# Optimization experiments

Measured on AMD Instinct MI355X. Metric: run time of the kernel, lower is better.

## Reference

```python
import jax, jax.numpy as jnp
import numpy as np

N_NODES = 50000
IN, HID, OUT = 128, 128, 47
N_EDGES = 800000


def _glorot(key, shape):
    fan_in, fan_out = shape[1], shape[0]
    lim = np.sqrt(6.0 / (fan_in + fan_out)).astype(np.float32)
    return jax.random.uniform(key, shape, jnp.float32, -lim, lim)


def setup_inputs() -> dict:
    key = jax.random.key(0)
    ks = jax.random.split(key, 12)
    x = jax.random.normal(ks[0], (N_NODES, IN), jnp.float32)
    src = jax.random.randint(ks[1], (N_EDGES,), 0, N_NODES)
    dst = jax.random.randint(ks[2], (N_EDGES,), 0, N_NODES)
    return {
        "x": x, "src": src, "dst": dst,
        "w_self1": _glorot(ks[3], (HID, IN)),  "w_neigh1": _glorot(ks[4], (HID, IN)),  "b1": jnp.zeros((HID,), jnp.float32),
        "w_self2": _glorot(ks[5], (HID, HID)), "w_neigh2": _glorot(ks[6], (HID, HID)), "b2": jnp.zeros((HID,), jnp.float32),
        "w_self3": _glorot(ks[7], (OUT, HID)), "w_neigh3": _glorot(ks[8], (OUT, HID)), "b3": jnp.zeros((OUT,), jnp.float32),
    }


def _sage_conv(h, src, dst, w_self, w_neigh, b):
    # gather src features, mean-reduce per dst node (DGL copy_u + mean)
    msg = h[src]                                                  # [E, d]
    agg = jax.ops.segment_sum(msg, dst, num_segments=N_NODES)    # [N, d]
    deg = jax.ops.segment_sum(jnp.ones((dst.shape[0],), h.dtype), dst, num_segments=N_NODES)
    mean = agg / jnp.maximum(deg, 1.0)[:, None]
    # DGL SAGEConv('mean'): fc_self(h_dst) + fc_neigh(h_neigh); bias on fc_self only
    return h @ w_self.T + b + mean @ w_neigh.T


def reference(x, src, dst,
              w_self1, w_neigh1, b1,
              w_self2, w_neigh2, b2,
              w_self3, w_neigh3, b3):
    h = _sage_conv(x, src, dst, w_self1, w_neigh1, b1)
    h = jax.nn.relu(h)  # dropout is identity in eval mode
    h = _sage_conv(h, src, dst, w_self2, w_neigh2, b2)
    h = jax.nn.relu(h)
    h = _sage_conv(h, src, dst, w_self3, w_neigh3, b3)
    return h
```

## Files before the change

kernel.cpp:

```cpp
#include <hip/hip_runtime.h>

#define N_NODES 50000
#define N_EDGES 800000
#define DIM 128
#define OUTD 47
#define NBK 196
#define EPB 4096
#define NBIN ((N_EDGES + EPB - 1) / EPB)
#define XCVT_NB (N_NODES * DIM / 8 / 256)
#define WCVT_NB (DIM + DIM + 48)

typedef __attribute__((ext_vector_type(8))) short v8s;
typedef __attribute__((ext_vector_type(8))) unsigned short v8u;
typedef __attribute__((ext_vector_type(4))) float v4f;
typedef __attribute__((ext_vector_type(2))) float v2f;

static __device__ __forceinline__ unsigned short f2bf(float f) {
    union { float f; unsigned int u; } v; v.f = f;
    unsigned int x = v.u;
    return (unsigned short)((x + 0x7fffu + ((x >> 16) & 1u)) >> 16);
}
static __device__ __forceinline__ unsigned char f2fp8(float f) {
    unsigned int pk = __builtin_amdgcn_cvt_pk_fp8_f32(f, f, 0, false);
    return (unsigned char)(pk & 0xffu);
}

__global__ __launch_bounds__(256) void k_prep(const float* __restrict__ x,
                                              unsigned short* __restrict__ xb,
                                              unsigned int* __restrict__ x8,
                                              const int* __restrict__ dst,
                                              int* __restrict__ parts,
                                              const float* __restrict__ ws1, const float* __restrict__ wn1,
                                              const float* __restrict__ ws2, const float* __restrict__ wn2,
                                              const float* __restrict__ ws3, const float* __restrict__ wn3,
                                              unsigned short* __restrict__ wb1,
                                              unsigned short* __restrict__ wb2,
                                              unsigned short* __restrict__ wb3) {
    __shared__ int hist[NBK];
    const int bx = blockIdx.x, tid = threadIdx.x;
    if (bx < XCVT_NB) {
        int i = bx * 256 + tid;
        float4 v0 = ((const float4*)x)[i * 2];
        float4 v1 = ((const float4*)x)[i * 2 + 1];
        ushort4 o0, o1;
        o0.x = f2bf(v0.x); o0.y = f2bf(v0.y); o0.z = f2bf(v0.z); o0.w = f2bf(v0.w);
        o1.x = f2bf(v1.x); o1.y = f2bf(v1.y); o1.z = f2bf(v1.z); o1.w = f2bf(v1.w);
        ((ushort4*)xb)[i * 2] = o0;
        ((ushort4*)xb)[i * 2 + 1] = o1;
        unsigned int a = __builtin_amdgcn_cvt_pk_fp8_f32(v0.x, v0.y, 0, false);
        a = __builtin_amdgcn_cvt_pk_fp8_f32(v0.z, v0.w, a, true);
        unsigned int b = __builtin_amdgcn_cvt_pk_fp8_f32(v1.x, v1.y, 0, false);
        b = __builtin_amdgcn_cvt_pk_fp8_f32(v1.z, v1.w, b, true);
        uint2 o; o.x = a; o.y = b;
        ((uint2*)x8)[i] = o;
    } else if (bx < XCVT_NB + NBIN) {
        const int j = bx - XCVT_NB;
        for (int i = tid; i < NBK; i += 256) hist[i] = 0;
        __syncthreads();
        const int e0 = j * EPB;
        const int ecnt = min(EPB, N_EDGES - e0);
        for (int r = tid; r < ecnt; r += 256)
            atomicAdd(&hist[dst[e0 + r] >> 8], 1);
        __syncthreads();
        for (int i = tid; i < NBK; i += 256) parts[j * NBK + i] = hist[i];
    } else {
        int b2 = bx - XCVT_NB - NBIN;
        const float *sw, *nw; unsigned short* ob; int j, J;
        if (b2 < DIM)            { sw = ws1; nw = wn1; ob = wb1; j = b2;            J = DIM; }
        else if (b2 < 2 * DIM)   { sw = ws2; nw = wn2; ob = wb2; j = b2 - DIM;      J = DIM; }
        else                     { sw = ws3; nw = wn3; ob = wb3; j = b2 - 2 * DIM;  J = OUTD; }
        int k = tid;
        float v = 0.f;
        if (j < J) v = (k < DIM) ? sw[j * DIM + k] : nw[j * DIM + (k - DIM)];
        ob[j * 256 + k] = f2bf(v);
    }
}

__global__ __launch_bounds__(256) void k_scan2(const int* __restrict__ parts,
                                               int* __restrict__ gbase,
                                               int* __restrict__ boffB,
                                               int* __restrict__ btot,
                                               int* __restrict__ row_ptr) {
    __shared__ int s[256];
    const int t = threadIdx.x;
    int tot = 0;
    if (t < NBK)
        for (int i = 0; i < NBIN; ++i) tot += parts[i * NBK + t];
    s[t] = tot;
    __syncthreads();
    for (int off = 1; off < 256; off <<= 1) {
        int u = (t >= off) ? s[t - off] : 0;
        __syncthreads();
        s[t] += u;
        __syncthreads();
    }
    if (t < NBK) {
        int run = s[t] - tot;
        boffB[t] = run; btot[t] = tot;
        for (int i = 0; i < NBIN; ++i) {
            gbase[i * NBK + t] = run;
            run += parts[i * NBK + t];
        }
    }
    if (t == 255) row_ptr[N_NODES] = s[255];
}

__global__ __launch_bounds__(256) void k_bin(const int* __restrict__ src,
                                             const int* __restrict__ dst,
                                             const int* __restrict__ gbase,
                                             unsigned int* __restrict__ packed) {
    __shared__ int gb[NBK], cnt[NBK];
    const int t = threadIdx.x;
    for (int i = t; i < NBK; i += 256) { gb[i] = gbase[blockIdx.x * NBK + i]; cnt[i] = 0; }
    __syncthreads();
    const int e0 = blockIdx.x * EPB;
    const int ecnt = min(EPB, N_EDGES - e0);
    for (int r = t; r < ecnt; r += 256) {
        int s = src[e0 + r], d = dst[e0 + r];
        int b = d >> 8;
        int loc = atomicAdd(&cnt[b], 1);
        packed[gb[b] + loc] = ((unsigned int)s << 8) | (unsigned int)(d & 255);
    }
}

__global__ __launch_bounds__(256) void k_place(const unsigned int* __restrict__ packed,
                                               const int* __restrict__ boffB,
                                               const int* __restrict__ btot,
                                               int* __restrict__ row_ptr,
                                               int* __restrict__ src_sorted) {
    __shared__ int hist[256], cur[256], s[256];
    const int b = blockIdx.x, t = threadIdx.x;
    hist[t] = 0;
    __syncthreads();
    const int base = boffB[b], cb = btot[b];
    for (int i = t; i < cb; i += 256)
        atomicAdd(&hist[packed[base + i] & 255u], 1);
    __syncthreads();
    int v = hist[t];
    s[t] = v;
    __syncthreads();
    for (int off = 1; off < 256; off <<= 1) {
        int u = (t >= off) ? s[t - off] : 0;
        __syncthreads();
        s[t] += u;
        __syncthreads();
    }
    int excl = base + s[t] - v;
    int node = b * 256 + t;
    if (node < N_NODES) row_ptr[node] = excl;
    cur[t] = excl;
    __syncthreads();
    for (int i = t; i < cb; i += 256) {
        unsigned int pkt = packed[base + i];
        int pos = atomicAdd(&cur[pkt & 255u], 1);
        src_sorted[pos] = (int)(pkt >> 8);
    }
}

__global__ __launch_bounds__(256) void k_agg8(const unsigned char* __restrict__ h8,
                                              const int* __restrict__ row_ptr,
                                              const int* __restrict__ srcs,
                                              unsigned short* __restrict__ meanb) {
    const int tid = threadIdx.x;
    const int lane = tid & 63, wv = tid >> 6;
    const int g = lane & 15, ns = lane >> 4;
    const int n = blockIdx.x * 16 + wv * 4 + ns;
    const int start = row_ptr[n], end = row_ptr[n + 1];
    float a0=0.f,a1=0.f,a2=0.f,a3=0.f,a4=0.f,a5=0.f,a6=0.f,a7=0.f;
    int e = start;
    for (; e + 2 <= end; e += 2) {
        int s0 = srcs[e], s1 = srcs[e + 1];
        uint2 u0 = *(const uint2*)(h8 + (size_t)s0 * DIM + g * 8);
        uint2 u1 = *(const uint2*)(h8 + (size_t)s1 * DIM + g * 8);
        v2f p0 = __builtin_amdgcn_cvt_pk_f32_fp8(u0.x, false);
        v2f p1 = __builtin_amdgcn_cvt_pk_f32_fp8(u0.x, true);
        v2f p2 = __builtin_amdgcn_cvt_pk_f32_fp8(u0.y, false);
        v2f p3 = __builtin_amdgcn_cvt_pk_f32_fp8(u0.y, true);
        v2f q0 = __builtin_amdgcn_cvt_pk_f32_fp8(u1.x, false);
        v2f q1 = __builtin_amdgcn_cvt_pk_f32_fp8(u1.x, true);
        v2f q2 = __builtin_amdgcn_cvt_pk_f32_fp8(u1.y, false);
        v2f q3 = __builtin_amdgcn_cvt_pk_f32_fp8(u1.y, true);
        a0 += p0[0] + q0[0]; a1 += p0[1] + q0[1];
        a2 += p1[0] + q1[0]; a3 += p1[1] + q1[1];
        a4 += p2[0] + q2[0]; a5 += p2[1] + q2[1];
        a6 += p3[0] + q3[0]; a7 += p3[1] + q3[1];
    }
    if (e < end) {
        int s0 = srcs[e];
        uint2 u0 = *(const uint2*)(h8 + (size_t)s0 * DIM + g * 8);
        v2f p0 = __builtin_amdgcn_cvt_pk_f32_fp8(u0.x, false);
        v2f p1 = __builtin_amdgcn_cvt_pk_f32_fp8(u0.x, true);
        v2f p2 = __builtin_amdgcn_cvt_pk_f32_fp8(u0.y, false);
        v2f p3 = __builtin_amdgcn_cvt_pk_f32_fp8(u0.y, true);
        a0 += p0[0]; a1 += p0[1]; a2 += p1[0]; a3 += p1[1];
        a4 += p2[0]; a5 += p2[1]; a6 += p3[0]; a7 += p3[1];
    }
    int d = end - start;
    float inv = (d > 0) ? 1.f / (float)d : 0.f;
    v8u o;
    o[0]=f2bf(a0*inv); o[1]=f2bf(a1*inv); o[2]=f2bf(a2*inv); o[3]=f2bf(a3*inv);
    o[4]=f2bf(a4*inv); o[5]=f2bf(a5*inv); o[6]=f2bf(a6*inv); o[7]=f2bf(a7*inv);
    *(v8u*)(meanb + (size_t)n * DIM + g * 8) = o;
}

template <int JT, int TPW, bool RELU, bool OUTBF>
__global__ __launch_bounds__(256) void k_gemm_lds(const unsigned short* __restrict__ Ab,
                                                  const unsigned short* __restrict__ Mb,
                                                  const unsigned short* __restrict__ Wb,
                                                  const float* __restrict__ bias,
                                                  void* __restrict__ out,
                                                  unsigned char* __restrict__ out8,
                                                  int outdim) {
    __shared__ unsigned short Alds[64 * 256];
    __shared__ unsigned short Wlds[JT * 256];
    const int tid = threadIdx.x;
    const int m0 = blockIdx.x * 64;
    const int j0 = blockIdx.y * JT;
    v8u ar[8];
    #pragma unroll
    for (int i = 0; i < 8; ++i) {
        int t = tid + 256 * i;
        int row = t >> 5, ch = t & 31;
        int node = m0 + row; if (node >= N_NODES) node = N_NODES - 1;
        const unsigned short* s = (ch < 16) ? (Ab + (size_t)node * DIM + ch * 8)
                                            : (Mb + (size_t)node * DIM + (ch - 16) * 8);
        ar[i] = *(const v8u*)s;
    }
    constexpr int WI = (JT * 32 + 255) / 256;
    v8u wr[WI];
    #pragma unroll
    for (int i = 0; i < WI; ++i) {
        int t = tid + 256 * i;
        if (t < JT * 32) {
            int row = t >> 5, ch = t & 31;
            wr[i] = *(const v8u*)(Wb + (size_t)(j0 + row) * 256 + ch * 8);
        }
    }
    #pragma unroll
    for (int i = 0; i < 8; ++i) {
        int t = tid + 256 * i;
        int row = t >> 5, ch = t & 31;
        *(v8u*)(Alds + row * 256 + ((ch * 8) ^ ((row & 7) * 8))) = ar[i];
    }
    #pragma unroll
    for (int i = 0; i < WI; ++i) {
        int t = tid + 256 * i;
        if (t < JT * 32) {
            int row = t >> 5, ch = t & 31;
            *(v8u*)(Wlds + row * 256 + ((ch * 8) ^ ((row & 7) * 8))) = wr[i];
        }
    }
    __syncthreads();
    const int lane = tid & 63, wv = tid >> 6;
    const int m = lane & 15, qd = lane >> 4;
    const int arow = wv * 16 + m;
    v4f acc[TPW] = {};
    #pragma unroll
    for (int c = 0; c < 8; ++c) {
        const int koff = c * 32 + qd * 8;
        v8s af = *(const v8s*)(Alds + arow * 256 + (koff ^ ((arow & 7) * 8)));
        #pragma unroll
        for (int t = 0; t < TPW; ++t) {
            int wrow = t * 16 + m;
            v8s wf = *(const v8s*)(Wlds + wrow * 256 + (koff ^ ((wrow & 7) * 8)));
            acc[t] = __builtin_amdgcn_mfma_f32_16x16x32_bf16(af, wf, acc[t], 0, 0, 0);
        }
    }
    #pragma unroll
    for (int t = 0; t < TPW; ++t) {
        int col = j0 + t * 16 + m;
        bool colok = (col < outdim);
        float bv = colok ? bias[col] : 0.f;
        #pragma unroll
        for (int r = 0; r < 4; ++r) {
            int nrow = m0 + wv * 16 + qd * 4 + r;
            if (colok && nrow < N_NODES) {
                float v = acc[t][r] + bv;
                if (RELU) v = fmaxf(v, 0.f);
                size_t idx = (size_t)nrow * outdim + col;
                if (OUTBF) {
                    ((unsigned short*)out)[idx] = f2bf(v);
                    out8[idx] = f2fp8(v);
                } else {
                    ((float*)out)[idx] = v;
                }
            }
        }
    }
}

extern "C" void kernel_launch(void* const* d_in, const int* in_sizes, int n_in,
                              void* d_out, int out_size, void* d_ws, size_t ws_size,
                              hipStream_t stream) {
    const float* x   = (const float*)d_in[0];
    const int*   src = (const int*)d_in[1];
    const int*   dst = (const int*)d_in[2];
    const float* ws1 = (const float*)d_in[3];
    const float* wn1 = (const float*)d_in[4];
    const float* b1  = (const float*)d_in[5];
    const float* ws2 = (const float*)d_in[6];
    const float* wn2 = (const float*)d_in[7];
    const float* b2  = (const float*)d_in[8];
    const float* ws3 = (const float*)d_in[9];
    const float* wn3 = (const float*)d_in[10];
    const float* b3  = (const float*)d_in[11];

    char* p = (char*)d_ws;
    auto alloc = [&](size_t bytes) { char* r = p; p += (bytes + 255) & ~(size_t)255; return r; };
    int*   row_ptr = (int*)alloc((size_t)(N_NODES + 1) * 4);
    int*   srcs    = (int*)alloc((size_t)N_EDGES * 4);
    unsigned int* packed = (unsigned int*)alloc((size_t)N_EDGES * 4);
    int*   parts   = (int*)alloc((size_t)NBIN * NBK * 4);
    int*   gbase   = (int*)alloc((size_t)NBIN * NBK * 4);
    int*   boffB   = (int*)alloc((size_t)NBK * 4);
    int*   btot    = (int*)alloc((size_t)NBK * 4);
    unsigned short* xb    = (unsigned short*)alloc((size_t)N_NODES * DIM * 2);
    unsigned short* meanb = (unsigned short*)alloc((size_t)N_NODES * DIM * 2);
    unsigned short* h1b   = (unsigned short*)alloc((size_t)N_NODES * DIM * 2);
    unsigned short* h2b   = (unsigned short*)alloc((size_t)N_NODES * DIM * 2);
    unsigned char*  h8    = (unsigned char*)alloc((size_t)N_NODES * DIM);
    unsigned short* wb1 = (unsigned short*)alloc((size_t)DIM * 256 * 2);
    unsigned short* wb2 = (unsigned short*)alloc((size_t)DIM * 256 * 2);
    unsigned short* wb3 = (unsigned short*)alloc((size_t)48 * 256 * 2);

    k_prep<<<XCVT_NB + NBIN + WCVT_NB, 256, 0, stream>>>(
        x, xb, (unsigned int*)h8, dst, parts,
        ws1, wn1, ws2, wn2, ws3, wn3, wb1, wb2, wb3);
    k_scan2<<<1, 256, 0, stream>>>(parts, gbase, boffB, btot, row_ptr);
    k_bin<<<NBIN, 256, 0, stream>>>(src, dst, gbase, packed);
    k_place<<<NBK, 256, 0, stream>>>(packed, boffB, btot, row_ptr, srcs);

    const int MB = (N_NODES + 63) / 64;
    const int AB = N_NODES / 16;

    k_agg8<<<AB, 256, 0, stream>>>(h8, row_ptr, srcs, meanb);
    k_gemm_lds<64, 4, true, true><<<dim3(MB, 2), 256, 0, stream>>>(xb, meanb, wb1, b1, h1b, h8, DIM);
    k_agg8<<<AB, 256, 0, stream>>>(h8, row_ptr, srcs, meanb);
    k_gemm_lds<64, 4, true, true><<<dim3(MB, 2), 256, 0, stream>>>(h1b, meanb, wb2, b2, h2b, h8, DIM);
    k_agg8<<<AB, 256, 0, stream>>>(h8, row_ptr, srcs, meanb);
    k_gemm_lds<48, 3, false, false><<<dim3(MB, 1), 256, 0, stream>>>(h2b, meanb, wb3, b3, d_out, nullptr, OUTD);
}
```

Baseline: 264.4 us.

## Fuse neighbor mean aggregation into per-layer GEMM kernel via LDS

Merges the separate aggregation kernel and the GEMM kernel into one per-layer kernel. Each block gathers and averages neighbor fp8 features for its 64 nodes straight into the LDS A-tile, then loops over output-column halves reloading weights. This removes the bf16 mean buffer write and readback and half the kernel launches, and uses ping-pong fp8 buffers because the fused kernel reads and writes h8 in the same launch. In exchange the grid drops from 3125 aggregation blocks to 782 blocks with less gather parallelism per block, and the gather is serialized before the MFMA phase.

```diff
diff --git a/kernel.cpp b/kernel.cpp
--- a/kernel.cpp
+++ b/kernel.cpp
@@ -157,132 +157,128 @@
     }
 }
 
-__global__ __launch_bounds__(256) void k_agg8(const unsigned char* __restrict__ h8,
-                                              const int* __restrict__ row_ptr,
-                                              const int* __restrict__ srcs,
-                                              unsigned short* __restrict__ meanb) {
-    const int tid = threadIdx.x;
-    const int lane = tid & 63, wv = tid >> 6;
-    const int g = lane & 15, ns = lane >> 4;
-    const int n = blockIdx.x * 16 + wv * 4 + ns;
-    const int start = row_ptr[n], end = row_ptr[n + 1];
-    float a0=0.f,a1=0.f,a2=0.f,a3=0.f,a4=0.f,a5=0.f,a6=0.f,a7=0.f;
-    int e = start;
-    for (; e + 2 <= end; e += 2) {
-        int s0 = srcs[e], s1 = srcs[e + 1];
-        uint2 u0 = *(const uint2*)(h8 + (size_t)s0 * DIM + g * 8);
-        uint2 u1 = *(const uint2*)(h8 + (size_t)s1 * DIM + g * 8);
-        v2f p0 = __builtin_amdgcn_cvt_pk_f32_fp8(u0.x, false);
-        v2f p1 = __builtin_amdgcn_cvt_pk_f32_fp8(u0.x, true);
-        v2f p2 = __builtin_amdgcn_cvt_pk_f32_fp8(u0.y, false);
-        v2f p3 = __builtin_amdgcn_cvt_pk_f32_fp8(u0.y, true);
-        v2f q0 = __builtin_amdgcn_cvt_pk_f32_fp8(u1.x, false);
-        v2f q1 = __builtin_amdgcn_cvt_pk_f32_fp8(u1.x, true);
-        v2f q2 = __builtin_amdgcn_cvt_pk_f32_fp8(u1.y, false);
-        v2f q3 = __builtin_amdgcn_cvt_pk_f32_fp8(u1.y, true);
-        a0 += p0[0] + q0[0]; a1 += p0[1] + q0[1];
-        a2 += p1[0] + q1[0]; a3 += p1[1] + q1[1];
-        a4 += p2[0] + q2[0]; a5 += p2[1] + q2[1];
-        a6 += p3[0] + q3[0]; a7 += p3[1] + q3[1];
-    }
-    if (e < end) {
-        int s0 = srcs[e];
-        uint2 u0 = *(const uint2*)(h8 + (size_t)s0 * DIM + g * 8);
-        v2f p0 = __builtin_amdgcn_cvt_pk_f32_fp8(u0.x, false);
-        v2f p1 = __builtin_amdgcn_cvt_pk_f32_fp8(u0.x, true);
-        v2f p2 = __builtin_amdgcn_cvt_pk_f32_fp8(u0.y, false);
-        v2f p3 = __builtin_amdgcn_cvt_pk_f32_fp8(u0.y, true);
-        a0 += p0[0]; a1 += p0[1]; a2 += p1[0]; a3 += p1[1];
-        a4 += p2[0]; a5 += p2[1]; a6 += p3[0]; a7 += p3[1];
-    }
-    int d = end - start;
-    float inv = (d > 0) ? 1.f / (float)d : 0.f;
-    v8u o;
-    o[0]=f2bf(a0*inv); o[1]=f2bf(a1*inv); o[2]=f2bf(a2*inv); o[3]=f2bf(a3*inv);
-    o[4]=f2bf(a4*inv); o[5]=f2bf(a5*inv); o[6]=f2bf(a6*inv); o[7]=f2bf(a7*inv);
-    *(v8u*)(meanb + (size_t)n * DIM + g * 8) = o;
-}
-
-template <int JT, int TPW, bool RELU, bool OUTBF>
-__global__ __launch_bounds__(256) void k_gemm_lds(const unsigned short* __restrict__ Ab,
-                                                  const unsigned short* __restrict__ Mb,
-                                                  const unsigned short* __restrict__ Wb,
-                                                  const float* __restrict__ bias,
-                                                  void* __restrict__ out,
-                                                  unsigned char* __restrict__ out8,
-                                                  int outdim) {
+template <int JH, int NH, int TPW, bool RELU, bool OUTBF>
+__global__ __launch_bounds__(256) void k_layer(const unsigned short* __restrict__ selfb,
+                                               const unsigned char* __restrict__ h8in,
+                                               const unsigned short* __restrict__ Wb,
+                                               const float* __restrict__ bias,
+                                               const int* __restrict__ row_ptr,
+                                               const int* __restrict__ srcs,
+                                               void* __restrict__ out,
+                                               unsigned char* __restrict__ out8,
+                                               int outdim) {
     __shared__ unsigned short Alds[64 * 256];
-    __shared__ unsigned short Wlds[JT * 256];
+    __shared__ unsigned short Wlds[JH * 256];
     const int tid = threadIdx.x;
     const int m0 = blockIdx.x * 64;
-    const int j0 = blockIdx.y * JT;
-    v8u ar[8];
     #pragma unroll
-    for (int i = 0; i < 8; ++i) {
+    for (int i = 0; i < 4; ++i) {
+        int t = tid + 256 * i;
+        int row = t >> 4, ch = t & 15;
+        int node = m0 + row; if (node >= N_NODES) node = N_NODES - 1;
+        v8u v = *(const v8u*)(selfb + (size_t)node * DIM + ch * 8);
+        *(v8u*)(Alds + row * 256 + ((ch * 8) ^ ((row & 7) * 8))) = v;
+    }
+    {
+        const int g = tid & 15, sl = tid >> 4;
+        for (int k = 0; k < 4; ++k) {
+            int row = sl * 4 + k;
+            int n = m0 + row;
+            float a0=0.f,a1=0.f,a2=0.f,a3=0.f,a4=0.f,a5=0.f,a6=0.f,a7=0.f;
+            int d = 0;
+            if (n < N_NODES) {
+                int start = row_ptr[n], end = row_ptr[n + 1];
+                d = end - start;
+                int e = start;
+                for (; e + 2 <= end; e += 2) {
+                    int s0 = srcs[e], s1 = srcs[e + 1];
+                    uint2 u0 = *(const uint2*)(h8in + (size_t)s0 * DIM + g * 8);
+                    uint2 u1 = *(const uint2*)(h8in + (size_t)s1 * DIM + g * 8);
+                    v2f p0 = __builtin_amdgcn_cvt_pk_f32_fp8(u0.x, false);
+                    v2f p1 = __builtin_amdgcn_cvt_pk_f32_fp8(u0.x, true);
+                    v2f p2 = __builtin_amdgcn_cvt_pk_f32_fp8(u0.y, false);
+                    v2f p3 = __builtin_amdgcn_cvt_pk_f32_fp8(u0.y, true);
+                    v2f q0 = __builtin_amdgcn_cvt_pk_f32_fp8(u1.x, false);
+                    v2f q1 = __builtin_amdgcn_cvt_pk_f32_fp8(u1.x, true);
+                    v2f q2 = __builtin_amdgcn_cvt_pk_f32_fp8(u1.y, false);
+                    v2f q3 = __builtin_amdgcn_cvt_pk_f32_fp8(u1.y, true);
+                    a0 += p0[0] + q0[0]; a1 += p0[1] + q0[1];
+                    a2 += p1[0] + q1[0]; a3 += p1[1] + q1[1];
+                    a4 += p2[0] + q2[0]; a5 += p2[1] + q2[1];
+                    a6 += p3[0] + q3[0]; a7 += p3[1] + q3[1];
+                }
+                if (e < end) {
+                    int s0 = srcs[e];
+                    uint2 u0 = *(const uint2*)(h8in + (size_t)s0 * DIM + g * 8);
+                    v2f p0 = __builtin_amdgcn_cvt_pk_f32_fp8(u0.x, false);
+                    v2f p1 = __builtin_amdgcn_cvt_pk_f32_fp8(u0.x, true);
+                    v2f p2 = __builtin_amdgcn_cvt_pk_f32_fp8(u0.y, false);
+                    v2f p3 = __builtin_amdgcn_cvt_pk_f32_fp8(u0.y, true);
+                    a0 += p0[0]; a1 += p0[1]; a2 += p1[0]; a3 += p1[1];
+                    a4 += p2[0]; a5 += p2[1]; a6 += p3[0]; a7 += p3[1];
+                }
+            }
+            float inv = (d > 0) ? 1.f / (float)d : 0.f;
+            v8u o;
+            o[0]=f2bf(a0*inv); o[1]=f2bf(a1*inv); o[2]=f2bf(a2*inv); o[3]=f2bf(a3*inv);
+            o[4]=f2bf(a4*inv); o[5]=f2bf(a5*inv); o[6]=f2bf(a6*inv); o[7]=f2bf(a7*inv);
+            *(v8u*)(Alds + row * 256 + ((128 + g * 8) ^ ((row & 7) * 8))) = o;
+        }
+    }
+    #pragma unroll
+    for (int i = 0; i < JH / 8; ++i) {
         int t = tid + 256 * i;
         int row = t >> 5, ch = t & 31;
-        int node = m0 + row; if (node >= N_NODES) node = N_NODES - 1;
-        const unsigned short* s = (ch < 16) ? (Ab + (size_t)node * DIM + ch * 8)
-                                            : (Mb + (size_t)node * DIM + (ch - 16) * 8);
-        ar[i] = *(const v8u*)s;
-    }
-    constexpr int WI = (JT * 32 + 255) / 256;
-    v8u wr[WI];
-    #pragma unroll
-    for (int i = 0; i < WI; ++i) {
-        int t = tid + 256 * i;
-        if (t < JT * 32) {
-            int row = t >> 5, ch = t & 31;
-            wr[i] = *(const v8u*)(Wb + (size_t)(j0 + row) * 256 + ch * 8);
-        }
-    }
-    #pragma unroll
-    for (int i = 0; i < 8; ++i) {
-        int t = tid + 256 * i;
-        int row = t >> 5, ch = t & 31;
-        *(v8u*)(Alds + row * 256 + ((ch * 8) ^ ((row & 7) * 8))) = ar[i];
-    }
-    #pragma unroll
-    for (int i = 0; i < WI; ++i) {
-        int t = tid + 256 * i;
-        if (t < JT * 32) {
-            int row = t >> 5, ch = t & 31;
-            *(v8u*)(Wlds + row * 256 + ((ch * 8) ^ ((row & 7) * 8))) = wr[i];
-        }
+        v8u v = *(const v8u*)(Wb + (size_t)row * 256 + ch * 8);
+        *(v8u*)(Wlds + row * 256 + ((ch * 8) ^ ((row & 7) * 8))) = v;
     }
     __syncthreads();
     const int lane = tid & 63, wv = tid >> 6;
     const int m = lane & 15, qd = lane >> 4;
     const int arow = wv * 16 + m;
-    v4f acc[TPW] = {};
-    #pragma unroll
-    for (int c = 0; c < 8; ++c) {
-        const int koff = c * 32 + qd * 8;
-        v8s af = *(const v8s*)(Alds + arow * 256 + (koff ^ ((arow & 7) * 8)));
+    #pragma unroll 1
+    for (int h = 0; h < NH; ++h) {
+        if (h > 0) {
+            __syncthreads();
+            #pragma unroll
+            for (int i = 0; i < JH / 8; ++i) {
+                int t = tid + 256 * i;
+                int row = t >> 5, ch = t & 31;
+                v8u v = *(const v8u*)(Wb + (size_t)(h * JH + row) * 256 + ch * 8);
+                *(v8u*)(Wlds + row * 256 + ((ch * 8) ^ ((row & 7) * 8))) = v;
+            }
+            __syncthreads();
+        }
+        v4f acc[TPW] = {};
+        #pragma unroll
+        for (int c = 0; c < 8; ++c) {
+            const int koff = c * 32 + qd * 8;
+            v8s af = *(const v8s*)(Alds + arow * 256 + (koff ^ ((arow & 7) * 8)));
+            #pragma unroll
+            for (int t = 0; t < TPW; ++t) {
+                int wrow = t * 16 + m;
+                v8s wf = *(const v8s*)(Wlds + wrow * 256 + (koff ^ ((wrow & 7) * 8)));
+                acc[t] = __builtin_amdgcn_mfma_f32_16x16x32_bf16(af, wf, acc[t], 0, 0, 0);
+            }
+        }
         #pragma unroll
         for (int t = 0; t < TPW; ++t) {
-            int wrow = t * 16 + m;
-            v8s wf = *(const v8s*)(Wlds + wrow * 256 + (koff ^ ((wrow & 7) * 8)));
-            acc[t] = __builtin_amdgcn_mfma_f32_16x16x32_bf16(af, wf, acc[t], 0, 0, 0);
-        }
-    }
-    #pragma unroll
-    for (int t = 0; t < TPW; ++t) {
-        int col = j0 + t * 16 + m;
-        bool colok = (col < outdim);
-        float bv = colok ? bias[col] : 0.f;
-        #pragma unroll
-        for (int r = 0; r < 4; ++r) {
-            int nrow = m0 + wv * 16 + qd * 4 + r;
-            if (colok && nrow < N_NODES) {
-                float v = acc[t][r] + bv;
-                if (RELU) v = fmaxf(v, 0.f);
-                size_t idx = (size_t)nrow * outdim + col;
-                if (OUTBF) {
-                    ((unsigned short*)out)[idx] = f2bf(v);
-                    out8[idx] = f2fp8(v);
-                } else {
-                    ((float*)out)[idx] = v;
+            int col = h * JH + t * 16 + m;
+            bool colok = (col < outdim);
+            float bv = colok ? bias[col] : 0.f;
+            #pragma unroll
+            for (int r = 0; r < 4; ++r) {
+                int nrow = m0 + wv * 16 + qd * 4 + r;
+                if (colok && nrow < N_NODES) {
+                    float v = acc[t][r] + bv;
+                    if (RELU) v = fmaxf(v, 0.f);
+                    size_t idx = (size_t)nrow * outdim + col;
+                    if (OUTBF) {
+                        ((unsigned short*)out)[idx] = f2bf(v);
+                        out8[idx] = f2fp8(v);
+                    } else {
+                        ((float*)out)[idx] = v;
+                    }
                 }
             }
         }
@@ -314,29 +310,28 @@
     int*   gbase   = (int*)alloc((size_t)NBIN * NBK * 4);
     int*   boffB   = (int*)alloc((size_t)NBK * 4);
     int*   btot    = (int*)alloc((size_t)NBK * 4);
-    unsigned short* xb    = (unsigned short*)alloc((size_t)N_NODES * DIM * 2);
-    unsigned short* meanb = (unsigned short*)alloc((size_t)N_NODES * DIM * 2);
-    unsigned short* h1b   = (unsigned short*)alloc((size_t)N_NODES * DIM * 2);
-    unsigned short* h2b   = (unsigned short*)alloc((size_t)N_NODES * DIM * 2);
-    unsigned char*  h8    = (unsigned char*)alloc((size_t)N_NODES * DIM);
+    unsigned short* xb  = (unsigned short*)alloc((size_t)N_NODES * DIM * 2);
+    unsigned short* h1b = (unsigned short*)alloc((size_t)N_NODES * DIM * 2);
+    unsigned short* h2b = (unsigned short*)alloc((size_t)N_NODES * DIM * 2);
+    unsigned char*  h8a = (unsigned char*)alloc((size_t)N_NODES * DIM);
+    unsigned char*  h8b = (unsigned char*)alloc((size_t)N_NODES * DIM);
     unsigned short* wb1 = (unsigned short*)alloc((size_t)DIM * 256 * 2);
     unsigned short* wb2 = (unsigned short*)alloc((size_t)DIM * 256 * 2);
     unsigned short* wb3 = (unsigned short*)alloc((size_t)48 * 256 * 2);
 
     k_prep<<<XCVT_NB + NBIN + WCVT_NB, 256, 0, stream>>>(
-        x, xb, (unsigned int*)h8, dst, parts,
+        x, xb, (unsigned int*)h8a, dst, parts,
         ws1, wn1, ws2, wn2, ws3, wn3, wb1, wb2, wb3);
     k_scan2<<<1, 256, 0, stream>>>(parts, gbase, boffB, btot, row_ptr);
     k_bin<<<NBIN, 256, 0, stream>>>(src, dst, gbase, packed);
     k_place<<<NBK, 256, 0, stream>>>(packed, boffB, btot, row_ptr, srcs);
 
     const int MB = (N_NODES + 63) / 64;
-    const int AB = N_NODES / 16;
-
-    k_agg8<<<AB, 256, 0, stream>>>(h8, row_ptr, srcs, meanb);
-    k_gemm_lds<64, 4, true, true><<<dim3(MB, 2), 256, 0, stream>>>(xb, meanb, wb1, b1, h1b, h8, DIM);
-    k_agg8<<<AB, 256, 0, stream>>>(h8, row_ptr, srcs, meanb);
-    k_gemm_lds<64, 4, true, true><<<dim3(MB, 2), 256, 0, stream>>>(h1b, meanb, wb2, b2, h2b, h8, DIM);
-    k_agg8<<<AB, 256, 0, stream>>>(h8, row_ptr, srcs, meanb);
-    k_gemm_lds<48, 3, false, false><<<dim3(MB, 1), 256, 0, stream>>>(h2b, meanb, wb3, b3, d_out, nullptr, OUTD);
-}
+
+    k_layer<64, 2, 4, true, true><<<MB, 256, 0, stream>>>(
+        xb, h8a, wb1, b1, row_ptr, srcs, h1b, h8b, DIM);
+    k_layer<64, 2, 4, true, true><<<MB, 256, 0, stream>>>(
+        h1b, h8b, wb2, b2, row_ptr, srcs, h2b, h8a, DIM);
+    k_layer<48, 1, 3, false, false><<<MB, 256, 0, stream>>>(
+        h2b, h8a, wb3, b3, row_ptr, srcs, d_out, nullptr, OUTD);
+}
```

New measurement: 359.7 us. 36.0% more time.

## Fold single-block scan into bin/place kernels and unroll aggregation by four

Applied to the files above, without the earlier changes.

Removes the single-block k_scan2 launch. Each k_bin and k_place block now recomputes the bucket prefix sums redundantly from the parts histogram, so that serial one-block kernel and its extra launch disappear. The gather loop in k_agg8 is unrolled from two to four edges per iteration, putting more independent loads in flight. The cost is that every block re-reads the full parts array (196x196 ints) and runs its own scan.

```diff
diff --git a/kernel.cpp b/kernel.cpp
--- a/kernel.cpp
+++ b/kernel.cpp
@@ -76,17 +76,20 @@
     }
 }
 
-__global__ __launch_bounds__(256) void k_scan2(const int* __restrict__ parts,
-                                               int* __restrict__ gbase,
-                                               int* __restrict__ boffB,
-                                               int* __restrict__ btot,
-                                               int* __restrict__ row_ptr) {
-    __shared__ int s[256];
+__global__ __launch_bounds__(256) void k_bin(const int* __restrict__ src,
+                                             const int* __restrict__ dst,
+                                             const int* __restrict__ parts,
+                                             unsigned int* __restrict__ packed) {
+    __shared__ int s[256], gb[NBK], cnt[NBK];
     const int t = threadIdx.x;
-    int tot = 0;
-    if (t < NBK)
-        for (int i = 0; i < NBIN; ++i) tot += parts[i * NBK + t];
-    s[t] = tot;
+    const int j = blockIdx.x;
+    int ct = 0, cp = 0;
+    for (int i = 0; i < NBIN; ++i) {
+        int v = (t < NBK) ? parts[i * NBK + t] : 0;
+        if (i == j) cp = ct;
+        ct += v;
+    }
+    s[t] = ct;
     __syncthreads();
     for (int off = 1; off < 256; off <<= 1) {
         int u = (t >= off) ? s[t - off] : 0;
@@ -94,45 +97,40 @@
         s[t] += u;
         __syncthreads();
     }
-    if (t < NBK) {
-        int run = s[t] - tot;
-        boffB[t] = run; btot[t] = tot;
-        for (int i = 0; i < NBIN; ++i) {
-            gbase[i * NBK + t] = run;
-            run += parts[i * NBK + t];
-        }
-    }
-    if (t == 255) row_ptr[N_NODES] = s[255];
-}
-
-__global__ __launch_bounds__(256) void k_bin(const int* __restrict__ src,
-                                             const int* __restrict__ dst,
-                                             const int* __restrict__ gbase,
-                                             unsigned int* __restrict__ packed) {
-    __shared__ int gb[NBK], cnt[NBK];
-    const int t = threadIdx.x;
-    for (int i = t; i < NBK; i += 256) { gb[i] = gbase[blockIdx.x * NBK + i]; cnt[i] = 0; }
-    __syncthreads();
-    const int e0 = blockIdx.x * EPB;
+    if (t < NBK) { gb[t] = (s[t] - ct) + cp; cnt[t] = 0; }
+    __syncthreads();
+    const int e0 = j * EPB;
     const int ecnt = min(EPB, N_EDGES - e0);
     for (int r = t; r < ecnt; r += 256) {
-        int s = src[e0 + r], d = dst[e0 + r];
+        int sv = src[e0 + r], d = dst[e0 + r];
         int b = d >> 8;
         int loc = atomicAdd(&cnt[b], 1);
-        packed[gb[b] + loc] = ((unsigned int)s << 8) | (unsigned int)(d & 255);
+        packed[gb[b] + loc] = ((unsigned int)sv << 8) | (unsigned int)(d & 255);
     }
 }
 
 __global__ __launch_bounds__(256) void k_place(const unsigned int* __restrict__ packed,
-                                               const int* __restrict__ boffB,
-                                               const int* __restrict__ btot,
+                                               const int* __restrict__ parts,
                                                int* __restrict__ row_ptr,
                                                int* __restrict__ src_sorted) {
-    __shared__ int hist[256], cur[256], s[256];
+    __shared__ int s[256], baseL[NBK], totL[NBK];
+    __shared__ int hist[256], cur[256];
     const int b = blockIdx.x, t = threadIdx.x;
+    int ct = 0;
+    for (int i = 0; i < NBIN; ++i)
+        ct += (t < NBK) ? parts[i * NBK + t] : 0;
+    s[t] = ct;
     hist[t] = 0;
     __syncthreads();
-    const int base = boffB[b], cb = btot[b];
+    for (int off = 1; off < 256; off <<= 1) {
+        int u = (t >= off) ? s[t - off] : 0;
+        __syncthreads();
+        s[t] += u;
+        __syncthreads();
+    }
+    if (t < NBK) { baseL[t] = s[t] - ct; totL[t] = ct; }
+    __syncthreads();
+    const int base = baseL[b], cb = totL[b];
     for (int i = t; i < cb; i += 256)
         atomicAdd(&hist[packed[base + i] & 255u], 1);
     __syncthreads();
@@ -148,6 +146,7 @@
     int excl = base + s[t] - v;
     int node = b * 256 + t;
     if (node < N_NODES) row_ptr[node] = excl;
+    if (b == NBK - 1 && t == 255) row_ptr[N_NODES] = base + cb;
     cur[t] = excl;
     __syncthreads();
     for (int i = t; i < cb; i += 256) {
@@ -168,10 +167,12 @@
     const int start = row_ptr[n], end = row_ptr[n + 1];
     float a0=0.f,a1=0.f,a2=0.f,a3=0.f,a4=0.f,a5=0.f,a6=0.f,a7=0.f;
     int e = start;
-    for (; e + 2 <= end; e += 2) {
-        int s0 = srcs[e], s1 = srcs[e + 1];
+    for (; e + 4 <= end; e += 4) {
+        int s0 = srcs[e], s1 = srcs[e + 1], s2 = srcs[e + 2], s3 = srcs[e + 3];
         uint2 u0 = *(const uint2*)(h8 + (size_t)s0 * DIM + g * 8);
         uint2 u1 = *(const uint2*)(h8 + (size_t)s1 * DIM + g * 8);
+        uint2 u2 = *(const uint2*)(h8 + (size_t)s2 * DIM + g * 8);
+        uint2 u3 = *(const uint2*)(h8 + (size_t)s3 * DIM + g * 8);
         v2f p0 = __builtin_amdgcn_cvt_pk_f32_fp8(u0.x, false);
         v2f p1 = __builtin_amdgcn_cvt_pk_f32_fp8(u0.x, true);
         v2f p2 = __builtin_amdgcn_cvt_pk_f32_fp8(u0.y, false);
@@ -180,12 +181,24 @@
         v2f q1 = __builtin_amdgcn_cvt_pk_f32_fp8(u1.x, true);
         v2f q2 = __builtin_amdgcn_cvt_pk_f32_fp8(u1.y, false);
         v2f q3 = __builtin_amdgcn_cvt_pk_f32_fp8(u1.y, true);
-        a0 += p0[0] + q0[0]; a1 += p0[1] + q0[1];
-        a2 += p1[0] + q1[0]; a3 += p1[1] + q1[1];
-        a4 += p2[0] + q2[0]; a5 += p2[1] + q2[1];
-        a6 += p3[0] + q3[0]; a7 += p3[1] + q3[1];
-    }
-    if (e < end) {
+        v2f r0 = __builtin_amdgcn_cvt_pk_f32_fp8(u2.x, false);
+        v2f r1 = __builtin_amdgcn_cvt_pk_f32_fp8(u2.x, true);
+        v2f r2 = __builtin_amdgcn_cvt_pk_f32_fp8(u2.y, false);
+        v2f r3 = __builtin_amdgcn_cvt_pk_f32_fp8(u2.y, true);
+        v2f w0 = __builtin_amdgcn_cvt_pk_f32_fp8(u3.x, false);
+        v2f w1 = __builtin_amdgcn_cvt_pk_f32_fp8(u3.x, true);
+        v2f w2 = __builtin_amdgcn_cvt_pk_f32_fp8(u3.y, false);
+        v2f w3 = __builtin_amdgcn_cvt_pk_f32_fp8(u3.y, true);
+        a0 += (p0[0] + q0[0]) + (r0[0] + w0[0]);
+        a1 += (p0[1] + q0[1]) + (r0[1] + w0[1]);
+        a2 += (p1[0] + q1[0]) + (r1[0] + w1[0]);
+        a3 += (p1[1] + q1[1]) + (r1[1] + w1[1]);
+        a4 += (p2[0] + q2[0]) + (r2[0] + w2[0]);
+        a5 += (p2[1] + q2[1]) + (r2[1] + w2[1]);
+        a6 += (p3[0] + q3[0]) + (r3[0] + w3[0]);
+        a7 += (p3[1] + q3[1]) + (r3[1] + w3[1]);
+    }
+    for (; e < end; ++e) {
         int s0 = srcs[e];
         uint2 u0 = *(const uint2*)(h8 + (size_t)s0 * DIM + g * 8);
         v2f p0 = __builtin_amdgcn_cvt_pk_f32_fp8(u0.x, false);
@@ -311,9 +324,6 @@
     int*   srcs    = (int*)alloc((size_t)N_EDGES * 4);
     unsigned int* packed = (unsigned int*)alloc((size_t)N_EDGES * 4);
     int*   parts   = (int*)alloc((size_t)NBIN * NBK * 4);
-    int*   gbase   = (int*)alloc((size_t)NBIN * NBK * 4);
-    int*   boffB   = (int*)alloc((size_t)NBK * 4);
-    int*   btot    = (int*)alloc((size_t)NBK * 4);
     unsigned short* xb    = (unsigned short*)alloc((size_t)N_NODES * DIM * 2);
     unsigned short* meanb = (unsigned short*)alloc((size_t)N_NODES * DIM * 2);
     unsigned short* h1b   = (unsigned short*)alloc((size_t)N_NODES * DIM * 2);
@@ -326,9 +336,8 @@
     k_prep<<<XCVT_NB + NBIN + WCVT_NB, 256, 0, stream>>>(
         x, xb, (unsigned int*)h8, dst, parts,
         ws1, wn1, ws2, wn2, ws3, wn3, wb1, wb2, wb3);
-    k_scan2<<<1, 256, 0, stream>>>(parts, gbase, boffB, btot, row_ptr);
-    k_bin<<<NBIN, 256, 0, stream>>>(src, dst, gbase, packed);
-    k_place<<<NBK, 256, 0, stream>>>(packed, boffB, btot, row_ptr, srcs);
+    k_bin<<<NBIN, 256, 0, stream>>>(src, dst, parts, packed);
+    k_place<<<NBK, 256, 0, stream>>>(packed, parts, row_ptr, srcs);
 
     const int MB = (N_NODES + 63) / 64;
     const int AB = N_NODES / 16;
```

Result: no change. 261.1 us, median of 2 (-1.3%).
